# Kernel tuning notes

Hardware: AMD Instinct MI355X
Metric: run time of the kernel (lower is better)

Reference implementation:

```python
import jax, jax.numpy as jnp
import numpy as np

IMG = 416
NC = 80
B = 32
NOBJ = 20          # objects placed per image
K = 32             # fixed max GT boxes per image for ignore-mask IoU (>= NOBJ)
THR = 0.5
ANCHORS = np.array([[10,13],[16,30],[33,23],[30,61],[62,45],[59,119],
                    [116,90],[156,198],[373,326]], np.float32)


def _bce(logits, targets):
    # elementwise binary_cross_entropy_with_logits
    return jnp.maximum(logits, 0.0) - logits * targets + jnp.log1p(jnp.exp(-jnp.abs(logits)))


def _make_y_true(key, batch, G, nc, img, nobj):
    N = G * G * 3
    k1, k2, k3, k4 = jax.random.split(key, 4)
    idx = jax.random.randint(k1, (batch, nobj), 0, N)
    xy = jax.random.uniform(k2, (batch, nobj, 2), jnp.float32) * img
    wh = jax.random.uniform(k3, (batch, nobj, 2), jnp.float32) * 90.0 + 10.0
    cls = jax.random.randint(k4, (batch, nobj), 0, nc)
    y = jnp.zeros((batch, N, 5 + nc), jnp.float32)
    b = jnp.arange(batch)[:, None]
    y = y.at[b, idx, 0].set(xy[..., 0])
    y = y.at[b, idx, 1].set(xy[..., 1])
    y = y.at[b, idx, 2].set(wh[..., 0])
    y = y.at[b, idx, 3].set(wh[..., 1])
    y = y.at[b, idx, 4].set(1.0)
    y = y.at[b, idx, 5 + cls].set(1.0)
    return y.reshape(batch, G, G, 3, 5 + nc)


def setup_inputs() -> dict:
    key = jax.random.key(0)
    ks = jax.random.split(key, 6)
    inp = {}
    for i, G in enumerate([13, 26, 52]):
        inp[f"fm{i}"] = jax.random.normal(ks[i], (B, 3 * (5 + NC), G, G), jnp.float32)
        inp[f"yt{i}"] = _make_y_true(ks[3 + i], B, G, NC, IMG, NOBJ)
    inp["anchors"] = jnp.asarray(ANCHORS)
    return inp


def _predict_transform(fm, anchors3):
    batch, ch, G, _ = fm.shape
    A = 3
    stride = IMG // G
    bbox = 5 + NC
    # [B, A*bbox, G*G] -> [B, G*G, A*bbox] -> [B, G, G, A, bbox]
    p = fm.reshape(batch, A * bbox, G * G).transpose(0, 2, 1).reshape(batch, G, G, A, bbox)
    box_centers = jax.nn.sigmoid(p[..., 0:2])
    box_sizes_raw = p[..., 2:4]
    conf_logits = p[..., 4:5]
    prob_logits = p[..., 5:]
    ar = jnp.arange(G, dtype=fm.dtype)
    gy, gx = jnp.meshgrid(ar, ar, indexing='ij')       # row, col
    xy_offset = jnp.stack([gx, gy], axis=-1).reshape(G, G, 1, 2)
    box_centers = (box_centers + xy_offset) * stride
    box_sizes = jnp.exp(box_sizes_raw) * (anchors3 / stride) * stride
    boxes = jnp.concatenate([box_centers, box_sizes], axis=-1)
    return xy_offset, boxes, conf_logits, prob_logits


def _ignore_mask(boxes, yt):
    batch, G, _, A, _ = boxes.shape
    N = G * G * A
    pb = boxes.reshape(batch, N, 4)
    tb_all = yt[..., :4].reshape(batch, N, 4)
    obj = yt[..., 4].reshape(batch, N)
    vals, idx = jax.lax.top_k(obj, K)                  # pick up to K GT boxes
    valid = vals > 0                                    # [B,K]
    tb = jnp.take_along_axis(tb_all, idx[:, :, None], axis=1)  # [B,K,4]
    tb = jnp.where(valid[:, :, None], tb, 0.0)
    p_xy = pb[:, :, None, 0:2]; p_wh = pb[:, :, None, 2:4]     # [B,N,1,2]
    t_xy = tb[:, None, :, 0:2]; t_wh = tb[:, None, :, 2:4]     # [B,1,K,2]
    mins = jnp.maximum(p_xy - p_wh / 2.0, t_xy - t_wh / 2.0)
    maxs = jnp.minimum(p_xy + p_wh / 2.0, t_xy + t_wh / 2.0)
    iwh = jnp.maximum(maxs - mins, 0.0)
    inter = iwh[..., 0] * iwh[..., 1]                  # [B,N,K]
    p_area = p_wh[..., 0] * p_wh[..., 1]
    t_area = t_wh[..., 0] * t_wh[..., 1]
    iou = inter / (p_area + t_area - inter + 1e-10)
    iou = jnp.where(valid[:, None, :], iou, 0.0)
    best_iou = jnp.max(iou, axis=-1)                   # [B,N]
    ign = (best_iou < THR).astype(boxes.dtype)
    # original: images with no valid GT boxes keep ignore_mask = 0
    ign = jnp.where(jnp.any(valid, axis=-1)[:, None], ign, 0.0)
    return ign.reshape(batch, G, G, A, 1)


def _calculate_one(fm, yt, anchors3):
    G = fm.shape[2]
    batch = yt.shape[0]
    ratio = IMG / G
    xy_offset, boxes, conf_logits, prob_logits = _predict_transform(fm, anchors3)
    object_mask = yt[..., 4:5]
    ignore_mask = _ignore_mask(boxes, yt)
    true_xy = yt[..., 0:2] / ratio - xy_offset
    pred_xy = boxes[..., 0:2] / ratio - xy_offset
    true_tw = yt[..., 2:4] / anchors3
    pred_tw = boxes[..., 2:4] / anchors3
    true_tw = jnp.where(true_tw == 0.0, 1.0, true_tw)
    pred_tw = jnp.where(pred_tw == 0.0, 1.0, pred_tw)
    true_tw = jnp.log(jnp.clip(true_tw, 1e-9, 1e9))
    pred_tw = jnp.log(jnp.clip(pred_tw, 1e-9, 1e9))
    box_scale = 2.0 - (yt[..., 2:3] / IMG) * (yt[..., 3:4] / IMG)
    xy_loss = 5.0 * jnp.sum((true_xy - pred_xy) ** 2 * object_mask * box_scale) / batch
    wh_loss = 5.0 * jnp.sum((true_tw - pred_tw) ** 2 * object_mask * box_scale) / batch
    bce_conf = _bce(conf_logits, object_mask)
    conf_loss = object_mask * bce_conf + 0.5 * (1.0 - object_mask) * ignore_mask * bce_conf
    focal = jnp.abs(object_mask - jax.nn.sigmoid(conf_logits)) ** 2.0   # alpha=1, gamma=2
    conf_loss = jnp.sum(conf_loss * focal) / batch
    delta = 0.01
    label_target = (1.0 - delta) * yt[..., 5:] + delta / NC
    class_loss = jnp.sum(object_mask * _bce(prob_logits, label_target)) / batch
    return xy_loss, wh_loss, conf_loss, class_loss


def reference(fm0, fm1, fm2, yt0, yt1, yt2, anchors):
    anchor_groups = [anchors[6:9], anchors[3:6], anchors[0:3]]
    fms = [fm0, fm1, fm2]
    yts = [yt0, yt1, yt2]
    xy = wh = conf = prob = 0.0
    for fm, yt, a3 in zip(fms, yts, anchor_groups):
        l_xy, l_wh, l_conf, l_prob = _calculate_one(fm, yt, a3)
        xy = xy + l_xy; wh = wh + l_wh; conf = conf + l_conf; prob = prob + l_prob
    total = xy + wh + conf + prob
    return (total, xy, wh, conf, prob)
```

## Files before the change

kernel.cpp:

```cpp
#include <hip/hip_runtime.h>
#include <math.h>


constexpr int   NCLS  = 80;
constexpr int   PMAX  = 4;
constexpr int   SLOTS = 32;
constexpr float IMGF  = 416.0f;

constexpr int NBLK_COLLECT = 32 * (1 + 2 + 4);
constexpr int NBLK_CONF    = 96 + 288 + 1056;
constexpr int NPART        = NBLK_COLLECT + NBLK_CONF;

constexpr size_t OFF_CNT  = 0;
constexpr size_t OFF_PART = 1536;
constexpr size_t OFF_TGT  = OFF_PART + (size_t)NPART * 16;
constexpr size_t OFF_TGTN = OFF_TGT + (size_t)96 * PMAX * SLOTS * 16;

__device__ inline float sigmoidf_(float x) { return 1.0f / (1.0f + expf(-x)); }
__device__ inline float bcef_(float l, float t) {
    return fmaxf(l, 0.0f) - l * t + log1pf(expf(-fabsf(l)));
}

__global__ __launch_bounds__(512) void k_collect(
        const float* __restrict__ fm0, const float* __restrict__ fm1,
        const float* __restrict__ fm2,
        const float* __restrict__ yt0, const float* __restrict__ yt1,
        const float* __restrict__ yt2,
        const float* __restrict__ anch,
        int* __restrict__ cnt, float* __restrict__ tgt, int* __restrict__ tgtn,
        float4* __restrict__ part) {
    int bid = blockIdx.x, tid = threadIdx.x;
    int lane = tid & 63, wid = tid >> 6;
    int s, b, p, P, G;
    const float *yt, *fm;
    int anchoff;
    if (bid < 32)      { s = 0; b = bid;          p = 0;       P = 1; yt = yt0; fm = fm0; G = 13; anchoff = 6; }
    else if (bid < 96) { s = 1; int i = bid - 32; b = i >> 1; p = i & 1; P = 2; yt = yt1; fm = fm1; G = 26; anchoff = 3; }
    else               { s = 2; int i = bid - 96; b = i >> 2; p = i & 3; P = 4; yt = yt2; fm = fm2; G = 52; anchoff = 0; }
    int GG   = G * G;
    int GG3  = 3 * GG;
    int per  = (GG3 + P - 1) / P;
    int nbase = p * per;
    int count = min(per, GG3 - nbase);
    int nit  = (count + 511) / 512;
    int sb = s * 32 + b;
    float stridef = IMGF / (float)G;

    __shared__ int    s_wcnt[8];
    __shared__ int    s_base;
    __shared__ int    s_n[SLOTS];
    __shared__ float4 s_box[SLOTS];
    __shared__ float4 s_pw[8];
    if (tid == 0) s_base = 0;

    float obj[4];
    int   nn[4];
    #pragma unroll
    for (int it = 0; it < 4; ++it) {
        int c = it * 512 + tid;
        nn[it]  = nbase + c;
        obj[it] = 0.0f;
        if (c < count) obj[it] = yt[(size_t)(b * GG3 + nn[it]) * 85 + 4];
    }
    __syncthreads();

    for (int it = 0; it < nit; ++it) {
        bool pos = obj[it] > 0.5f;
        unsigned long long mask = __ballot(pos);
        if (lane == 0) s_wcnt[wid] = __popcll(mask);
        __syncthreads();
        int wpre = 0, tot = 0;
        #pragma unroll
        for (int w = 0; w < 8; ++w) { if (w < wid) wpre += s_wcnt[w]; tot += s_wcnt[w]; }
        int rank = s_base + wpre + (int)__popcll(mask & ((1ull << lane) - 1ull));
        if (pos && rank < SLOTS) {
            size_t yb = (size_t)(b * GG3 + nn[it]) * 85;
            int slot = (sb * PMAX + p) * SLOTS + rank;
            float4 box = make_float4(yt[yb], yt[yb + 1], yt[yb + 2], yt[yb + 3]);
            reinterpret_cast<float4*>(tgt)[slot] = box;
            tgtn[slot] = nn[it];
            s_box[rank] = box;
            s_n[rank]   = nn[it];
        }
        __syncthreads();
        if (tid == 0) s_base += tot;
        __syncthreads();
    }
    int cn = min(s_base, SLOTS);
    if (tid == 0) {
        cnt[sb * PMAX + p] = cn;
        if (p == 0)
            for (int q = P; q < PMAX; ++q) cnt[sb * PMAX + q] = 0;
    }

    float ax = 0.f, aw2 = 0.f, ap = 0.f;
    for (int slot = wid; slot < cn; slot += 8) {
        float4 tb = s_box[slot];
        int n  = s_n[slot];
        int a  = n % 3;
        int sp = n / 3;
        int jj = sp % G, ii = sp / G;
        int ybase = (b * GG3 + n) * 85;
        int fbase = (b * 255 + a * 85) * GG + sp;
        for (int c = lane; c < NCLS; c += 64) {
            float pl  = fm[fbase + (5 + c) * GG];
            float tl  = yt[ybase + 5 + c];
            float lab = 0.99f * tl + 1.25e-4f;
            ap += bcef_(pl, lab);
        }
        if (lane == 0) {
            float p0 = fm[fbase];
            float p1 = fm[fbase + GG];
            float p2 = fm[fbase + 2 * GG];
            float p3 = fm[fbase + 3 * GG];
            float bcx = (sigmoidf_(p0) + (float)jj) * stridef;
            float bcy = (sigmoidf_(p1) + (float)ii) * stridef;
            float predx = bcx / stridef - (float)jj;
            float predy = bcy / stridef - (float)ii;
            float truex = tb.x / stridef - (float)jj;
            float truey = tb.y / stridef - (float)ii;
            float dx = truex - predx, dy = truey - predy;
            float bscale = 2.0f - (tb.z / IMGF) * (tb.w / IMGF);
            float aw = anch[(anchoff + a) * 2], ah = anch[(anchoff + a) * 2 + 1];
            float pw = expf(p2) * (aw / stridef) * stridef;
            float ph = expf(p3) * (ah / stridef) * stridef;
            float ptw = pw / aw, pth = ph / ah;
            float ttw = tb.z / aw, tth = tb.w / ah;
            ttw = (ttw == 0.0f) ? 1.0f : ttw;
            tth = (tth == 0.0f) ? 1.0f : tth;
            ptw = (ptw == 0.0f) ? 1.0f : ptw;
            pth = (pth == 0.0f) ? 1.0f : pth;
            ttw = logf(fminf(fmaxf(ttw, 1e-9f), 1e9f));
            tth = logf(fminf(fmaxf(tth, 1e-9f), 1e9f));
            ptw = logf(fminf(fmaxf(ptw, 1e-9f), 1e9f));
            pth = logf(fminf(fmaxf(pth, 1e-9f), 1e9f));
            float dw = ttw - ptw, dh = tth - pth;
            ax  += (dx * dx + dy * dy) * bscale;
            aw2 += (dw * dw + dh * dh) * bscale;
        }
    }
    for (int off = 32; off; off >>= 1) ap += __shfl_down(ap, off);
    if (lane == 0) s_pw[wid] = make_float4(ax, aw2, ap, 0.f);
    __syncthreads();
    if (tid == 0) {
        float X = 0.f, W = 0.f, Pp = 0.f;
        #pragma unroll
        for (int w = 0; w < 8; ++w) { X += s_pw[w].x; W += s_pw[w].y; Pp += s_pw[w].z; }
        part[bid] = make_float4(X, W, Pp, 0.f);
    }
}

__global__ __launch_bounds__(256) void k_conf(
        const float* __restrict__ fm0, const float* __restrict__ fm1,
        const float* __restrict__ fm2,
        const float* __restrict__ anch,
        const int* __restrict__ cnt, const float* __restrict__ tgt,
        const int* __restrict__ tgtn, float4* __restrict__ part) {
    __shared__ float  s_minx[128], s_maxx[128], s_miny[128], s_maxy[128], s_area[128];
    __shared__ int    s_tn[128];
    __shared__ int    s_cn4[4];
    __shared__ float  s_w1[4];

    int bid = blockIdx.x;
    int tid = threadIdx.x;
    int wid = tid >> 6, lane = tid & 63;

    int cb = bid;
    const float *fm;
    int G, chunks, s, anchoff;
    if (cb < 96)       { fm = fm0; G = 13; chunks = 1;  s = 0; anchoff = 6; }
    else if (cb < 384) { cb -= 96;  fm = fm1; G = 26; chunks = 3;  s = 1; anchoff = 3; }
    else               { cb -= 384; fm = fm2; G = 52; chunks = 11; s = 2; anchoff = 0; }
    int chunk = cb % chunks;
    int ba    = cb / chunks;
    int b = ba / 3, a = ba % 3;
    int GG = G * G;
    float stridef = IMGF / (float)G;
    int sb = s * 32 + b;
    if (tid < 4) s_cn4[tid] = cnt[sb * PMAX + tid];
    if (tid < 128) {
        int slot = sb * PMAX * SLOTS + tid;
        float4 tb = reinterpret_cast<const float4*>(tgt)[slot];
        s_minx[tid] = tb.x - tb.z * 0.5f;
        s_maxx[tid] = tb.x + tb.z * 0.5f;
        s_miny[tid] = tb.y - tb.w * 0.5f;
        s_maxy[tid] = tb.y + tb.w * 0.5f;
        s_area[tid] = tb.z * tb.w;
        s_tn[tid]   = tgtn[slot];
    }
    __syncthreads();

    float ac = 0.f;
    int sp = chunk * 256 + tid;
    if (sp < GG) {
        int jj = sp % G, ii = sp / G;
        int n = sp * 3 + a;
        int fbase = (b * 255 + a * 85) * GG + sp;
        float p0 = fm[fbase];
        float p1 = fm[fbase + GG];
        float p2 = fm[fbase + 2 * GG];
        float p3 = fm[fbase + 3 * GG];
        float p4 = fm[fbase + 4 * GG];
        float aw = anch[(anchoff + a) * 2], ah = anch[(anchoff + a) * 2 + 1];
        float cx = (sigmoidf_(p0) + (float)jj) * stridef;
        float cy = (sigmoidf_(p1) + (float)ii) * stridef;
        float pw = expf(p2) * (aw / stridef) * stridef;
        float ph = expf(p3) * (ah / stridef) * stridef;
        float pminx = cx - pw * 0.5f, pmaxx = cx + pw * 0.5f;
        float pminy = cy - ph * 0.5f, pmaxy = cy + ph * 0.5f;
        float parea = pw * ph;
        float best = 0.0f, m = 0.0f;
        int cn_total = 0;
        #pragma unroll
        for (int pp = 0; pp < PMAX; ++pp) {
            int cnp = s_cn4[pp];
            cn_total += cnp;
            for (int k = 0; k < cnp; ++k) {
                int e = pp * SLOTS + k;
                if (s_tn[e] == n) m = 1.0f;
                float iw = fminf(pmaxx, s_maxx[e]) - fmaxf(pminx, s_minx[e]);
                float ih = fminf(pmaxy, s_maxy[e]) - fmaxf(pminy, s_miny[e]);
                iw = fmaxf(iw, 0.0f);
                ih = fmaxf(ih, 0.0f);
                float inter = iw * ih;
                float iou = inter / ((parea + s_area[e] - inter) + 1e-10f);
                best = fmaxf(best, iou);
            }
        }
        float ign = (cn_total > 0 && best < 0.5f) ? 1.0f : 0.0f;
        float bce = bcef_(p4, m);
        float d = fabsf(m - sigmoidf_(p4));
        ac = (m * bce + 0.5f * (1.0f - m) * ign * bce) * (d * d);
    }

    for (int off = 32; off; off >>= 1) ac += __shfl_down(ac, off);
    if (lane == 0) s_w1[wid] = ac;
    __syncthreads();
    if (tid == 0)
        part[NBLK_COLLECT + bid] =
            make_float4(0.f, 0.f, 0.f, s_w1[0] + s_w1[1] + s_w1[2] + s_w1[3]);
}

__global__ __launch_bounds__(512) void k_reduce(
        const float4* __restrict__ part, float* __restrict__ out) {
    int t = threadIdx.x;
    double x = 0.0, w = 0.0, p = 0.0, c = 0.0;
    for (int i = t; i < NPART; i += 512) {
        float4 v = part[i];
        x += (double)v.x; w += (double)v.y; p += (double)v.z; c += (double)v.w;
    }
    for (int off = 32; off; off >>= 1) {
        x += __shfl_down(x, off);
        w += __shfl_down(w, off);
        p += __shfl_down(p, off);
        c += __shfl_down(c, off);
    }
    __shared__ double sx[8], sw[8], sp[8], sc[8];
    int wid = t >> 6, lane = t & 63;
    if (lane == 0) { sx[wid] = x; sw[wid] = w; sp[wid] = p; sc[wid] = c; }
    __syncthreads();
    if (t == 0) {
        double X = 0, W = 0, P = 0, C = 0;
        for (int i = 0; i < 8; ++i) { X += sx[i]; W += sw[i]; P += sp[i]; C += sc[i]; }
        double xy = 5.0 * X / 32.0;
        double wh = 5.0 * W / 32.0;
        double cf = C / 32.0;
        double pb = P / 32.0;
        out[0] = (float)(xy + wh + cf + pb);
        out[1] = (float)xy;
        out[2] = (float)wh;
        out[3] = (float)cf;
        out[4] = (float)pb;
    }
}

extern "C" void kernel_launch(void* const* d_in, const int* in_sizes, int n_in,
                              void* d_out, int out_size, void* d_ws, size_t ws_size,
                              hipStream_t stream) {
    const float* fm0  = (const float*)d_in[0];
    const float* yt0  = (const float*)d_in[1];
    const float* fm1  = (const float*)d_in[2];
    const float* yt1  = (const float*)d_in[3];
    const float* fm2  = (const float*)d_in[4];
    const float* yt2  = (const float*)d_in[5];
    const float* anch = (const float*)d_in[6];
    float* out = (float*)d_out;

    char* ws = (char*)d_ws;
    int*    cnt  = (int*)(ws + OFF_CNT);
    float4* part = (float4*)(ws + OFF_PART);
    float*  tgt  = (float*)(ws + OFF_TGT);
    int*    tgtn = (int*)(ws + OFF_TGTN);

    k_collect<<<NBLK_COLLECT, 512, 0, stream>>>(
        fm0, fm1, fm2, yt0, yt1, yt2, anch, cnt, tgt, tgtn, part);
    k_conf<<<NBLK_CONF, 256, 0, stream>>>(
        fm0, fm1, fm2, anch, cnt, tgt, tgtn, part);
    k_reduce<<<1, 512, 0, stream>>>(part, out);
}
```

Measured before the change: 34.42 us.

## Fuse target collection and confidence loss into one per-image kernel

Merges the collect and conf kernels into a single kernel with one 1024-thread block per (scale, image). Each block gathers its GT boxes into shared memory and then computes the confidence/ignore loss directly, removing the global tgt/cnt round trip and one launch. It also reads the object mask from registers instead of matching target indices. The cost is far less parallelism: 96 large blocks instead of about 1600, with the 52x52 blocks serially doing 8 iterations each, so load imbalance and low occupancy could dominate.

```diff
diff --git a/kernel.cpp b/kernel.cpp
--- a/kernel.cpp
+++ b/kernel.cpp
@@ -2,99 +2,83 @@
 #include <math.h>
 
 
-constexpr int   NCLS  = 80;
-constexpr int   PMAX  = 4;
-constexpr int   SLOTS = 32;
-constexpr float IMGF  = 416.0f;
-
-constexpr int NBLK_COLLECT = 32 * (1 + 2 + 4);
-constexpr int NBLK_CONF    = 96 + 288 + 1056;
-constexpr int NPART        = NBLK_COLLECT + NBLK_CONF;
-
-constexpr size_t OFF_CNT  = 0;
-constexpr size_t OFF_PART = 1536;
-constexpr size_t OFF_TGT  = OFF_PART + (size_t)NPART * 16;
-constexpr size_t OFF_TGTN = OFF_TGT + (size_t)96 * PMAX * SLOTS * 16;
+constexpr int   NCLS = 80;
+constexpr int   KMAX = 32;
+constexpr float IMGF = 416.0f;
+
 
 __device__ inline float sigmoidf_(float x) { return 1.0f / (1.0f + expf(-x)); }
 __device__ inline float bcef_(float l, float t) {
     return fmaxf(l, 0.0f) - l * t + log1pf(expf(-fabsf(l)));
 }
 
-__global__ __launch_bounds__(512) void k_collect(
-        const float* __restrict__ fm0, const float* __restrict__ fm1,
-        const float* __restrict__ fm2,
-        const float* __restrict__ yt0, const float* __restrict__ yt1,
-        const float* __restrict__ yt2,
-        const float* __restrict__ anch,
-        int* __restrict__ cnt, float* __restrict__ tgt, int* __restrict__ tgtn,
-        float4* __restrict__ part) {
-    int bid = blockIdx.x, tid = threadIdx.x;
-    int lane = tid & 63, wid = tid >> 6;
-    int s, b, p, P, G;
-    const float *yt, *fm;
-    int anchoff;
-    if (bid < 32)      { s = 0; b = bid;          p = 0;       P = 1; yt = yt0; fm = fm0; G = 13; anchoff = 6; }
-    else if (bid < 96) { s = 1; int i = bid - 32; b = i >> 1; p = i & 1; P = 2; yt = yt1; fm = fm1; G = 26; anchoff = 3; }
-    else               { s = 2; int i = bid - 96; b = i >> 2; p = i & 3; P = 4; yt = yt2; fm = fm2; G = 52; anchoff = 0; }
-    int GG   = G * G;
-    int GG3  = 3 * GG;
-    int per  = (GG3 + P - 1) / P;
-    int nbase = p * per;
-    int count = min(per, GG3 - nbase);
-    int nit  = (count + 511) / 512;
-    int sb = s * 32 + b;
-    float stridef = IMGF / (float)G;
-
-    __shared__ int    s_wcnt[8];
+template<int G, int NIT>
+__device__ void run_sb(const float* __restrict__ fm, const float* __restrict__ yt,
+                       const float* __restrict__ anch, int aoff,
+                       int b, int bid, float4* __restrict__ part) {
+    constexpr int GG  = G * G;
+    constexpr int GG3 = 3 * GG;
+    const float stridef = IMGF / (float)G;
+    const int tid  = threadIdx.x;
+    const int lane = tid & 63, wid = tid >> 6;
+
+    __shared__ int    s_wcnt[16];
     __shared__ int    s_base;
-    __shared__ int    s_n[SLOTS];
-    __shared__ float4 s_box[SLOTS];
-    __shared__ float4 s_pw[8];
+    __shared__ int    s_n[KMAX];
+    __shared__ float4 s_box[KMAX];
+    __shared__ float  s_minx[KMAX], s_maxx[KMAX], s_miny[KMAX], s_maxy[KMAX], s_area[KMAX];
+    __shared__ float4 s_w[16];
     if (tid == 0) s_base = 0;
 
-    float obj[4];
-    int   nn[4];
+    float obj[NIT];
     #pragma unroll
-    for (int it = 0; it < 4; ++it) {
-        int c = it * 512 + tid;
-        nn[it]  = nbase + c;
+    for (int it = 0; it < NIT; ++it) {
+        int c = it * 1024 + tid;
         obj[it] = 0.0f;
-        if (c < count) obj[it] = yt[(size_t)(b * GG3 + nn[it]) * 85 + 4];
-    }
-    __syncthreads();
-
-    for (int it = 0; it < nit; ++it) {
+        if (c < GG3) {
+            int a = c / GG, sp = c - a * GG;
+            int n = sp * 3 + a;
+            obj[it] = yt[(size_t)(b * GG3 + n) * 85 + 4];
+        }
+    }
+    __syncthreads();
+
+    #pragma unroll
+    for (int it = 0; it < NIT; ++it) {
         bool pos = obj[it] > 0.5f;
         unsigned long long mask = __ballot(pos);
         if (lane == 0) s_wcnt[wid] = __popcll(mask);
         __syncthreads();
         int wpre = 0, tot = 0;
         #pragma unroll
-        for (int w = 0; w < 8; ++w) { if (w < wid) wpre += s_wcnt[w]; tot += s_wcnt[w]; }
+        for (int w = 0; w < 16; ++w) { int v = s_wcnt[w]; if (w < wid) wpre += v; tot += v; }
         int rank = s_base + wpre + (int)__popcll(mask & ((1ull << lane) - 1ull));
-        if (pos && rank < SLOTS) {
-            size_t yb = (size_t)(b * GG3 + nn[it]) * 85;
-            int slot = (sb * PMAX + p) * SLOTS + rank;
-            float4 box = make_float4(yt[yb], yt[yb + 1], yt[yb + 2], yt[yb + 3]);
-            reinterpret_cast<float4*>(tgt)[slot] = box;
-            tgtn[slot] = nn[it];
-            s_box[rank] = box;
-            s_n[rank]   = nn[it];
+        if (pos && rank < KMAX) {
+            int c = it * 1024 + tid;
+            int a = c / GG, sp = c - a * GG;
+            int n = sp * 3 + a;
+            size_t yb = (size_t)(b * GG3 + n) * 85;
+            s_box[rank] = make_float4(yt[yb], yt[yb + 1], yt[yb + 2], yt[yb + 3]);
+            s_n[rank]   = n;
         }
         __syncthreads();
         if (tid == 0) s_base += tot;
         __syncthreads();
     }
-    int cn = min(s_base, SLOTS);
-    if (tid == 0) {
-        cnt[sb * PMAX + p] = cn;
-        if (p == 0)
-            for (int q = P; q < PMAX; ++q) cnt[sb * PMAX + q] = 0;
-    }
-
-    float ax = 0.f, aw2 = 0.f, ap = 0.f;
-    for (int slot = wid; slot < cn; slot += 8) {
+    int cn = min(s_base, KMAX);
+    if (tid < cn) {
+        float4 tb = s_box[tid];
+        s_minx[tid] = tb.x - tb.z * 0.5f;
+        s_maxx[tid] = tb.x + tb.z * 0.5f;
+        s_miny[tid] = tb.y - tb.w * 0.5f;
+        s_maxy[tid] = tb.y + tb.w * 0.5f;
+        s_area[tid] = tb.z * tb.w;
+    }
+    __syncthreads();
+
+    float ax = 0.f, aw2 = 0.f, ap = 0.f, ac = 0.f;
+
+    for (int slot = wid; slot < cn; slot += 16) {
         float4 tb = s_box[slot];
         int n  = s_n[slot];
         int a  = n % 3;
@@ -121,7 +105,7 @@
             float truey = tb.y / stridef - (float)ii;
             float dx = truex - predx, dy = truey - predy;
             float bscale = 2.0f - (tb.z / IMGF) * (tb.w / IMGF);
-            float aw = anch[(anchoff + a) * 2], ah = anch[(anchoff + a) * 2 + 1];
+            float aw = anch[(aoff + a) * 2], ah = anch[(aoff + a) * 2 + 1];
             float pw = expf(p2) * (aw / stridef) * stridef;
             float ph = expf(p3) * (ah / stridef) * stridef;
             float ptw = pw / aw, pth = ph / ah;
@@ -139,129 +123,87 @@
             aw2 += (dw * dw + dh * dh) * bscale;
         }
     }
-    for (int off = 32; off; off >>= 1) ap += __shfl_down(ap, off);
-    if (lane == 0) s_pw[wid] = make_float4(ax, aw2, ap, 0.f);
-    __syncthreads();
-    if (tid == 0) {
-        float X = 0.f, W = 0.f, Pp = 0.f;
-        #pragma unroll
-        for (int w = 0; w < 8; ++w) { X += s_pw[w].x; W += s_pw[w].y; Pp += s_pw[w].z; }
-        part[bid] = make_float4(X, W, Pp, 0.f);
-    }
-}
-
-__global__ __launch_bounds__(256) void k_conf(
-        const float* __restrict__ fm0, const float* __restrict__ fm1,
-        const float* __restrict__ fm2,
-        const float* __restrict__ anch,
-        const int* __restrict__ cnt, const float* __restrict__ tgt,
-        const int* __restrict__ tgtn, float4* __restrict__ part) {
-    __shared__ float  s_minx[128], s_maxx[128], s_miny[128], s_maxy[128], s_area[128];
-    __shared__ int    s_tn[128];
-    __shared__ int    s_cn4[4];
-    __shared__ float  s_w1[4];
-
-    int bid = blockIdx.x;
-    int tid = threadIdx.x;
-    int wid = tid >> 6, lane = tid & 63;
-
-    int cb = bid;
-    const float *fm;
-    int G, chunks, s, anchoff;
-    if (cb < 96)       { fm = fm0; G = 13; chunks = 1;  s = 0; anchoff = 6; }
-    else if (cb < 384) { cb -= 96;  fm = fm1; G = 26; chunks = 3;  s = 1; anchoff = 3; }
-    else               { cb -= 384; fm = fm2; G = 52; chunks = 11; s = 2; anchoff = 0; }
-    int chunk = cb % chunks;
-    int ba    = cb / chunks;
-    int b = ba / 3, a = ba % 3;
-    int GG = G * G;
-    float stridef = IMGF / (float)G;
-    int sb = s * 32 + b;
-    if (tid < 4) s_cn4[tid] = cnt[sb * PMAX + tid];
-    if (tid < 128) {
-        int slot = sb * PMAX * SLOTS + tid;
-        float4 tb = reinterpret_cast<const float4*>(tgt)[slot];
-        s_minx[tid] = tb.x - tb.z * 0.5f;
-        s_maxx[tid] = tb.x + tb.z * 0.5f;
-        s_miny[tid] = tb.y - tb.w * 0.5f;
-        s_maxy[tid] = tb.y + tb.w * 0.5f;
-        s_area[tid] = tb.z * tb.w;
-        s_tn[tid]   = tgtn[slot];
-    }
-    __syncthreads();
-
-    float ac = 0.f;
-    int sp = chunk * 256 + tid;
-    if (sp < GG) {
-        int jj = sp % G, ii = sp / G;
-        int n = sp * 3 + a;
-        int fbase = (b * 255 + a * 85) * GG + sp;
-        float p0 = fm[fbase];
-        float p1 = fm[fbase + GG];
-        float p2 = fm[fbase + 2 * GG];
-        float p3 = fm[fbase + 3 * GG];
-        float p4 = fm[fbase + 4 * GG];
-        float aw = anch[(anchoff + a) * 2], ah = anch[(anchoff + a) * 2 + 1];
-        float cx = (sigmoidf_(p0) + (float)jj) * stridef;
-        float cy = (sigmoidf_(p1) + (float)ii) * stridef;
-        float pw = expf(p2) * (aw / stridef) * stridef;
-        float ph = expf(p3) * (ah / stridef) * stridef;
-        float pminx = cx - pw * 0.5f, pmaxx = cx + pw * 0.5f;
-        float pminy = cy - ph * 0.5f, pmaxy = cy + ph * 0.5f;
-        float parea = pw * ph;
-        float best = 0.0f, m = 0.0f;
-        int cn_total = 0;
-        #pragma unroll
-        for (int pp = 0; pp < PMAX; ++pp) {
-            int cnp = s_cn4[pp];
-            cn_total += cnp;
-            for (int k = 0; k < cnp; ++k) {
-                int e = pp * SLOTS + k;
-                if (s_tn[e] == n) m = 1.0f;
-                float iw = fminf(pmaxx, s_maxx[e]) - fmaxf(pminx, s_minx[e]);
-                float ih = fminf(pmaxy, s_maxy[e]) - fmaxf(pminy, s_miny[e]);
+
+    #pragma unroll
+    for (int it = 0; it < NIT; ++it) {
+        int c = it * 1024 + tid;
+        if (c < GG3) {
+            int a = c / GG, sp = c - a * GG;
+            int n = sp * 3 + a;
+            (void)n;
+            int jj = sp % G, ii = sp / G;
+            int fbase = (b * 255 + a * 85) * GG + sp;
+            float p0 = fm[fbase];
+            float p1 = fm[fbase + GG];
+            float p2 = fm[fbase + 2 * GG];
+            float p3 = fm[fbase + 3 * GG];
+            float p4 = fm[fbase + 4 * GG];
+            float aw = anch[(aoff + a) * 2], ah = anch[(aoff + a) * 2 + 1];
+            float cx = (sigmoidf_(p0) + (float)jj) * stridef;
+            float cy = (sigmoidf_(p1) + (float)ii) * stridef;
+            float pw = expf(p2) * (aw / stridef) * stridef;
+            float ph = expf(p3) * (ah / stridef) * stridef;
+            float pminx = cx - pw * 0.5f, pmaxx = cx + pw * 0.5f;
+            float pminy = cy - ph * 0.5f, pmaxy = cy + ph * 0.5f;
+            float parea = pw * ph;
+            float best = 0.0f;
+            for (int k = 0; k < cn; ++k) {
+                float iw = fminf(pmaxx, s_maxx[k]) - fmaxf(pminx, s_minx[k]);
+                float ih = fminf(pmaxy, s_maxy[k]) - fmaxf(pminy, s_miny[k]);
                 iw = fmaxf(iw, 0.0f);
                 ih = fmaxf(ih, 0.0f);
                 float inter = iw * ih;
-                float iou = inter / ((parea + s_area[e] - inter) + 1e-10f);
+                float iou = inter / ((parea + s_area[k] - inter) + 1e-10f);
                 best = fmaxf(best, iou);
             }
-        }
-        float ign = (cn_total > 0 && best < 0.5f) ? 1.0f : 0.0f;
-        float bce = bcef_(p4, m);
-        float d = fabsf(m - sigmoidf_(p4));
-        ac = (m * bce + 0.5f * (1.0f - m) * ign * bce) * (d * d);
-    }
-
-    for (int off = 32; off; off >>= 1) ac += __shfl_down(ac, off);
-    if (lane == 0) s_w1[wid] = ac;
-    __syncthreads();
-    if (tid == 0)
-        part[NBLK_COLLECT + bid] =
-            make_float4(0.f, 0.f, 0.f, s_w1[0] + s_w1[1] + s_w1[2] + s_w1[3]);
-}
-
-__global__ __launch_bounds__(512) void k_reduce(
+            float m   = (obj[it] > 0.5f) ? 1.0f : 0.0f;
+            float ign = (cn > 0 && best < 0.5f) ? 1.0f : 0.0f;
+            float bce = bcef_(p4, m);
+            float d   = fabsf(m - sigmoidf_(p4));
+            ac += (m * bce + 0.5f * (1.0f - m) * ign * bce) * (d * d);
+        }
+    }
+
+    for (int off = 32; off; off >>= 1) {
+        ax  += __shfl_down(ax,  off);
+        aw2 += __shfl_down(aw2, off);
+        ap  += __shfl_down(ap,  off);
+        ac  += __shfl_down(ac,  off);
+    }
+    if (lane == 0) s_w[wid] = make_float4(ax, aw2, ap, ac);
+    __syncthreads();
+    if (tid == 0) {
+        float X = 0.f, W = 0.f, P = 0.f, C = 0.f;
+        #pragma unroll
+        for (int w = 0; w < 16; ++w) { X += s_w[w].x; W += s_w[w].y; P += s_w[w].z; C += s_w[w].w; }
+        part[bid] = make_float4(X, W, P, C);
+    }
+}
+
+__global__ __launch_bounds__(1024) void k_mega(
+        const float* __restrict__ fm0, const float* __restrict__ fm1,
+        const float* __restrict__ fm2,
+        const float* __restrict__ yt0, const float* __restrict__ yt1,
+        const float* __restrict__ yt2,
+        const float* __restrict__ anch, float4* __restrict__ part) {
+    int bid = blockIdx.x;
+    if (bid < 32)      run_sb<52, 8>(fm2, yt2, anch, 0, bid,      bid, part);
+    else if (bid < 64) run_sb<26, 2>(fm1, yt1, anch, 3, bid - 32, bid, part);
+    else               run_sb<13, 1>(fm0, yt0, anch, 6, bid - 64, bid, part);
+}
+
+__global__ __launch_bounds__(128) void k_reduce(
         const float4* __restrict__ part, float* __restrict__ out) {
+    __shared__ float4 s_p[96];
     int t = threadIdx.x;
-    double x = 0.0, w = 0.0, p = 0.0, c = 0.0;
-    for (int i = t; i < NPART; i += 512) {
-        float4 v = part[i];
-        x += (double)v.x; w += (double)v.y; p += (double)v.z; c += (double)v.w;
-    }
-    for (int off = 32; off; off >>= 1) {
-        x += __shfl_down(x, off);
-        w += __shfl_down(w, off);
-        p += __shfl_down(p, off);
-        c += __shfl_down(c, off);
-    }
-    __shared__ double sx[8], sw[8], sp[8], sc[8];
-    int wid = t >> 6, lane = t & 63;
-    if (lane == 0) { sx[wid] = x; sw[wid] = w; sp[wid] = p; sc[wid] = c; }
+    if (t < 96) s_p[t] = part[t];
     __syncthreads();
     if (t == 0) {
         double X = 0, W = 0, P = 0, C = 0;
-        for (int i = 0; i < 8; ++i) { X += sx[i]; W += sw[i]; P += sp[i]; C += sc[i]; }
+        for (int i = 0; i < 96; ++i) {
+            float4 v = s_p[i];
+            X += (double)v.x; W += (double)v.y; P += (double)v.z; C += (double)v.w;
+        }
         double xy = 5.0 * X / 32.0;
         double wh = 5.0 * W / 32.0;
         double cf = C / 32.0;
@@ -286,15 +228,8 @@
     const float* anch = (const float*)d_in[6];
     float* out = (float*)d_out;
 
-    char* ws = (char*)d_ws;
-    int*    cnt  = (int*)(ws + OFF_CNT);
-    float4* part = (float4*)(ws + OFF_PART);
-    float*  tgt  = (float*)(ws + OFF_TGT);
-    int*    tgtn = (int*)(ws + OFF_TGTN);
-
-    k_collect<<<NBLK_COLLECT, 512, 0, stream>>>(
-        fm0, fm1, fm2, yt0, yt1, yt2, anch, cnt, tgt, tgtn, part);
-    k_conf<<<NBLK_CONF, 256, 0, stream>>>(
-        fm0, fm1, fm2, anch, cnt, tgt, tgtn, part);
-    k_reduce<<<1, 512, 0, stream>>>(part, out);
-}
+    float4* part = (float4*)d_ws;
+
+    k_mega<<<96, 1024, 0, stream>>>(fm0, fm1, fm2, yt0, yt1, yt2, anch, part);
+    k_reduce<<<1, 128, 0, stream>>>(part, out);
+}
```

Result: slower. 84.91 us (+146.7%).
